# Kernel tuning notes

Measured on AMD Instinct MI355X. Metric: run time of the kernel, lower is better.

The kernel has to match this reference:

```python
import jax, jax.numpy as jnp
import numpy as np

DIM = 192
HEADS = 4
EPS = 1e-12  # F.normalize default eps


def setup_inputs() -> dict:
    key = jax.random.key(0)
    ks = jax.random.split(key, 5)
    b, c, h, w = 8, DIM, 128, 128
    x = jax.random.normal(ks[0], (b, c, h, w), dtype=jnp.float32)
    w_qkv = jax.random.normal(ks[1], (3 * DIM, DIM, 1, 1), dtype=jnp.float32) * (1.0 / np.sqrt(DIM))
    w_dw = jax.random.normal(ks[2], (3 * DIM, 1, 3, 3), dtype=jnp.float32) * (1.0 / 3.0)
    w_proj = jax.random.normal(ks[3], (DIM, DIM, 1, 1), dtype=jnp.float32) * (1.0 / np.sqrt(DIM))
    temperature = jnp.ones((HEADS, 1, 1), dtype=jnp.float32)
    return {"x": x, "w_qkv": w_qkv, "w_dw": w_dw, "w_proj": w_proj, "temperature": temperature}


def _conv1x1(x, w):
    # x: [b,c,h,w], w: [o,c,1,1] -> [b,o,h,w]
    return jnp.einsum('bchw,oc->bohw', x, w[:, :, 0, 0])


def _dwconv3x3(x, w):
    # depthwise 3x3, padding=1; x: [b,C,h,w], w: [C,1,3,3]
    C = x.shape[1]
    return jax.lax.conv_general_dilated(
        x, w, window_strides=(1, 1), padding=((1, 1), (1, 1)),
        dimension_numbers=('NCHW', 'OIHW', 'NCHW'), feature_group_count=C)


def _l2norm(x):
    n = jnp.linalg.norm(x, axis=-1, keepdims=True)
    return x / jnp.maximum(n, EPS)


def reference(x, w_qkv, w_dw, w_proj, temperature):
    b, c, h, w = x.shape
    head = HEADS
    ch = c // head  # channels per head
    qkv = _dwconv3x3(_conv1x1(x, w_qkv), w_dw)  # [b, 3c, h, w]
    q, k, v = jnp.split(qkv, 3, axis=1)  # each [b, c, h, w]

    def to_heads(t):
        # b (head ch) h w -> b head h (ch w)
        t = t.reshape(b, head, ch, h, w)
        return t.transpose(0, 1, 3, 2, 4).reshape(b, head, h, ch * w)

    q1 = _l2norm(to_heads(q))
    k1 = _l2norm(to_heads(k))
    v1 = to_heads(v)
    # attn over height dim: [b, head, h, h]
    attn = jax.nn.softmax(jnp.einsum('bhif,bhjf->bhij', q1, k1) * temperature[None], axis=-1)
    out = jnp.einsum('bhij,bhjf->bhif', attn, v1)  # [b, head, h, ch*w]
    # b head h (ch w) -> b (head ch) h w
    out = out.reshape(b, head, h, ch, w).transpose(0, 1, 3, 2, 4).reshape(b, c, h, w)
    return _conv1x1(out, w_proj)
```

## Files before the change

kernel.cpp:

```cpp
#include <hip/hip_runtime.h>
#include <hip/hip_bf16.h>

#define BB 8
#define CC 192
#define C3 576
#define NH 4
#define CH 48
#define HH 128
#define WW 128
#define HW 16384
#define FF 6144

typedef short s16x8 __attribute__((ext_vector_type(8)));
typedef float f32x4 __attribute__((ext_vector_type(4)));

constexpr size_t SPM = 32ull * 128 * 128;

constexpr size_t OFF_XT  = 0;
constexpr size_t SZ_XT   = (size_t)BB * HW * CC * 2;
constexpr size_t OFF_WQ  = OFF_XT + SZ_XT;
constexpr size_t SZ_WQ   = (size_t)C3 * CC * 2;
constexpr size_t OFF_WP  = OFF_WQ + SZ_WQ;
constexpr size_t SZ_WP   = (size_t)CC * CC * 2;
constexpr size_t OFF_RAW = OFF_WP + SZ_WP;
constexpr size_t SZ_RAW  = (size_t)BB * C3 * HW * 2;
constexpr size_t OFF_DW  = OFF_RAW + SZ_RAW;
constexpr size_t OFF_SP  = OFF_DW + SZ_RAW;
constexpr size_t OFF_ATB = OFF_SP + 8 * SPM * 4;
constexpr size_t OFF_RQ  = OFF_ATB + 32ull * 128 * 128 * 2;
constexpr size_t OFF_RK  = OFF_RQ + 32 * 128 * 4;
constexpr size_t OFF_PS  = OFF_SP;

__device__ __forceinline__ void store_out(__hip_bfloat16* p, float v) { *p = __float2bfloat16(v); }
__device__ __forceinline__ void store_out(float* p, float v) { *p = v; }

__device__ __forceinline__ short bf16bits(float v) {
  __hip_bfloat16 t = __float2bfloat16(v);
  return *reinterpret_cast<short*>(&t);
}
__device__ __forceinline__ float b2f(short u) {
  union { unsigned int i; float f; } x;
  x.i = ((unsigned int)(unsigned short)u) << 16;
  return x.f;
}

__device__ __forceinline__ void gload16(const void* g, void* l) {
  __builtin_amdgcn_global_load_lds((const __attribute__((address_space(1))) unsigned int*)g,
                                   (__attribute__((address_space(3))) unsigned int*)l, 16, 0, 0);
}

__global__ __launch_bounds__(256) void k_cvt_t(const float* __restrict__ in,
                                               __hip_bfloat16* __restrict__ outT) {
  const int p0 = blockIdx.x * 64;
  const int c0 = blockIdx.y * 32;
  const int b = blockIdx.z;
  __shared__ float t[32][65];
  const float* ib = in + (size_t)b * CC * HW;
  const int tid = threadIdx.x;
  {
    const int c = tid >> 3, pl = (tid & 7) * 8;
    const float* s = ib + (size_t)(c0 + c) * HW + p0 + pl;
#pragma unroll
    for (int j = 0; j < 8; ++j) t[c][pl + j] = s[j];
  }
  __syncthreads();
  {
    const int pl = tid >> 2, cl = (tid & 3) * 8;
    __hip_bfloat16* d = outT + (size_t)b * HW * CC + (size_t)(p0 + pl) * CC + c0 + cl;
#pragma unroll
    for (int j = 0; j < 8; ++j) d[j] = __float2bfloat16(t[cl + j][pl]);
  }
}

__global__ __launch_bounds__(256) void k_cvt_w(const float* __restrict__ in,
                                               __hip_bfloat16* __restrict__ out, int n) {
  const int i = blockIdx.x * 256 + threadIdx.x;
  if (i < n) out[i] = __float2bfloat16(in[i]);
}

template <int M, typename OutT>
__global__ __launch_bounds__(256) void k_gemm(const __hip_bfloat16* __restrict__ xT,
                                              const __hip_bfloat16* __restrict__ Wb,
                                              OutT* __restrict__ out) {
  const int pBase = blockIdx.x * 128;
  const int mBase = blockIdx.y * 192;
  const int b = blockIdx.z;
  __shared__ __hip_bfloat16 Al[6144];
  __shared__ __hip_bfloat16 Bl[4096];
  const int tid = threadIdx.x;
  const int wave = tid >> 6, lane = tid & 63;
  const int wm = wave >> 1, wn = wave & 1;
  const __hip_bfloat16* xb = xT + (size_t)b * HW * CC;
  char* Alc = (char*)Al;
  char* Blc = (char*)Bl;
  f32x4 acc[6][4] = {};

  for (int k0 = 0; k0 < CC; k0 += 32) {
#pragma unroll
    for (int is = 0; is < 3; ++is) {
      const int ci = is * 256 + tid;
      const int row = ci & 15, kg = (ci >> 4) & 3, mf = ci >> 6;
      gload16(Wb + (size_t)(mBase + mf * 16 + row) * CC + k0 + kg * 8,
              Alc + is * 4096 + wave * 1024);
    }
#pragma unroll
    for (int is = 0; is < 2; ++is) {
      const int ci = is * 256 + tid;
      const int col = ci & 15, kg = (ci >> 4) & 3, nf = ci >> 6;
      gload16(xb + (size_t)(pBase + nf * 16 + col) * CC + k0 + kg * 8,
              Blc + is * 4096 + wave * 1024);
    }
    __syncthreads();
    s16x8 a[6], bf[4];
#pragma unroll
    for (int i = 0; i < 6; ++i) a[i] = *(const s16x8*)(Alc + ((wm * 6 + i) << 10) + (lane << 4));
#pragma unroll
    for (int j = 0; j < 4; ++j) bf[j] = *(const s16x8*)(Blc + ((wn * 4 + j) << 10) + (lane << 4));
#pragma unroll
    for (int i = 0; i < 6; ++i)
#pragma unroll
      for (int j = 0; j < 4; ++j)
        acc[i][j] = __builtin_amdgcn_mfma_f32_16x16x32_bf16(a[i], bf[j], acc[i][j], 0, 0, 0);
    __syncthreads();
  }
  OutT* ob = out + (size_t)b * M * HW;
  const int r0 = (lane >> 4) * 4, cl = lane & 15;
#pragma unroll
  for (int i = 0; i < 6; ++i) {
    const int o = mBase + (wm * 6 + i) * 16 + r0;
#pragma unroll
    for (int j = 0; j < 4; ++j) {
      const int p = pBase + (wn * 4 + j) * 16 + cl;
      OutT* dst = ob + (size_t)o * HW + p;
#pragma unroll
      for (int r = 0; r < 4; ++r) store_out(dst + (size_t)r * HW, acc[i][j][r]);
    }
  }
}

__global__ __launch_bounds__(256) void k_dwconv(const __hip_bfloat16* __restrict__ in,
                                                const float* __restrict__ wdw,
                                                __hip_bfloat16* __restrict__ out,
                                                __hip_bfloat16* __restrict__ vt,
                                                float* __restrict__ psum) {
  const int h0 = blockIdx.x * 32;
  const int c = blockIdx.y;
  const int b = blockIdx.z;
  __shared__ __hip_bfloat16 IN[34][152];
  __shared__ char TR[8192];
  const int tid = threadIdx.x;
  const __hip_bfloat16* src = in + ((size_t)b * C3 + c) * HW;
  if (tid < 68) {
    const int r = tid >> 1, col = (tid & 1) ? 136 : 0;
    *(s16x8*)(&IN[r][col]) = (s16x8){};
  }
#pragma unroll
  for (int it = 0; it < 3; ++it) {
    const int vi = it * 256 + tid;
    if (vi < 544) {
      const int r = vi >> 4, w8 = vi & 15;
      const int hg = h0 - 1 + r;
      s16x8 v = {};
      if (hg >= 0 && hg < HH) v = *(const s16x8*)(src + (size_t)hg * WW + w8 * 8);
      *(s16x8*)(&IN[r][8 + w8 * 8]) = v;
    }
  }
  const float* wp = wdw + c * 9;
  float wgt[9];
#pragma unroll
  for (int q = 0; q < 9; ++q) wgt[q] = wp[q];
  __syncthreads();

  const int hl = tid >> 3, w0 = (tid & 7) * 16;
  float res[16] = {};
#pragma unroll
  for (int dh = 0; dh < 3; ++dh) {
    const __hip_bfloat16* rp = &IN[hl + dh][0];
    const s16x8 v0 = *(const s16x8*)(rp + w0);
    const s16x8 v1 = *(const s16x8*)(rp + w0 + 8);
    const s16x8 v2 = *(const s16x8*)(rp + w0 + 16);
    const s16x8 v3 = *(const s16x8*)(rp + w0 + 24);
    float rv[18];
    rv[0] = b2f(v0[7]);
#pragma unroll
    for (int e = 0; e < 8; ++e) rv[1 + e] = b2f(v1[e]);
#pragma unroll
    for (int e = 0; e < 8; ++e) rv[9 + e] = b2f(v2[e]);
    rv[17] = b2f(v3[0]);
    const float wa = wgt[dh * 3], wb = wgt[dh * 3 + 1], wc = wgt[dh * 3 + 2];
#pragma unroll
    for (int ww = 0; ww < 16; ++ww)
      res[ww] += rv[ww] * wa + rv[ww + 1] * wb + rv[ww + 2] * wc;
  }
  if (c < 2 * CC) {
    short pk[16];
#pragma unroll
    for (int ww = 0; ww < 16; ++ww) pk[ww] = bf16bits(res[ww]);
    __hip_bfloat16* dst = out + ((size_t)b * C3 + c) * HW + (size_t)(h0 + hl) * WW + w0;
    *(s16x8*)dst = *(const s16x8*)pk;
    *(s16x8*)(dst + 8) = *(const s16x8*)(pk + 8);
    float ss = 0.f;
#pragma unroll
    for (int ww = 0; ww < 16; ++ww) ss += res[ww] * res[ww];
#pragma unroll
    for (int off = 4; off > 0; off >>= 1) ss += __shfl_down(ss, off);
    if ((tid & 7) == 0) psum[((size_t)b * HH + h0 + hl) * 384 + c] = ss;
  } else {
    const int rel = c - 2 * CC;
    const int hd = rel / CH, ch = rel - hd * CH;
#pragma unroll
    for (int ww = 0; ww < 16; ++ww) {
      const int w = w0 + ww;
      const int blk = ((w << 2) + (hl >> 3)) ^ ((w >> 3) & 3);
      *(short*)(TR + (blk << 4) + ((hl & 7) << 1)) = bf16bits(res[ww]);
    }
    __syncthreads();
    const int w = tid >> 1, hf = tid & 1;
    short ot[16];
#pragma unroll
    for (int j = 0; j < 2; ++j) {
      const int hh = hf * 16 + j * 8;
      const int blk = ((w << 2) + (hh >> 3)) ^ ((w >> 3) & 3);
      *(s16x8*)(ot + j * 8) = *(const s16x8*)(TR + (blk << 4));
    }
    __hip_bfloat16* vd = vt + ((size_t)(b * NH + hd) * FF + (size_t)ch * WW + w) * HH + h0 + hf * 16;
    *(s16x8*)vd = *(const s16x8*)ot;
    *(s16x8*)(vd + 8) = *(const s16x8*)(ot + 8);
  }
}

__global__ __launch_bounds__(64) void k_norms2(const float* __restrict__ psum,
                                               float* __restrict__ rq, float* __restrict__ rk) {
  const int i = blockIdx.x;
  const int hd = blockIdx.y;
  const int b = blockIdx.z & 7;
  const int which = blockIdx.z >> 3;
  const int lane = threadIdx.x;
  float s = 0.f;
  if (lane < 48) s = psum[((size_t)b * HH + i) * 384 + which * CC + hd * CH + lane];
#pragma unroll
  for (int off = 32; off > 0; off >>= 1) s += __shfl_down(s, off);
  if (lane == 0) {
    const float n = sqrtf(s);
    float* dst = which ? rk : rq;
    dst[(b * NH + hd) * HH + i] = 1.f / fmaxf(n, 1e-12f);
  }
}

__global__ __launch_bounds__(256) void k_qkm(const __hip_bfloat16* __restrict__ dw,
                                             float* __restrict__ sp) {
  const int ks = blockIdx.x;
  const int bh = blockIdx.y;
  const int b = bh >> 2, hd = bh & 3;
  const __hip_bfloat16* qb = dw + ((size_t)b * C3 + hd * CH) * HW;
  const __hip_bfloat16* kb = dw + ((size_t)b * C3 + CC + hd * CH) * HW;
  __shared__ __hip_bfloat16 Al[4096];
  __shared__ __hip_bfloat16 Bl[4096];
  char* Alc = (char*)Al;
  char* Blc = (char*)Bl;
  const int tid = threadIdx.x, wave = tid >> 6, lane = tid & 63;
  const int wm = wave >> 1, wn = wave & 1;
  f32x4 acc[4][4] = {};
  for (int chunk = 0; chunk < 24; ++chunk) {
    const int ch = ks * 6 + (chunk >> 2);
    const int w0 = (chunk & 3) * 32;
#pragma unroll
    for (int is = 0; is < 2; ++is) {
      const int ci = is * 256 + tid;
      const int row = ci & 15, kg = (ci >> 4) & 3, mf = ci >> 6;
      gload16(qb + (size_t)ch * HW + (mf * 16 + row) * WW + w0 + kg * 8,
              Alc + is * 4096 + wave * 1024);
    }
#pragma unroll
    for (int is = 0; is < 2; ++is) {
      const int ci = is * 256 + tid;
      const int col = ci & 15, kg = (ci >> 4) & 3, nf = ci >> 6;
      gload16(kb + (size_t)ch * HW + (nf * 16 + col) * WW + w0 + kg * 8,
              Blc + is * 4096 + wave * 1024);
    }
    __syncthreads();
    s16x8 a[4], bf[4];
#pragma unroll
    for (int i = 0; i < 4; ++i) a[i] = *(const s16x8*)(Alc + ((wm * 4 + i) << 10) + (lane << 4));
#pragma unroll
    for (int j = 0; j < 4; ++j) bf[j] = *(const s16x8*)(Blc + ((wn * 4 + j) << 10) + (lane << 4));
#pragma unroll
    for (int i = 0; i < 4; ++i)
#pragma unroll
      for (int j = 0; j < 4; ++j)
        acc[i][j] = __builtin_amdgcn_mfma_f32_16x16x32_bf16(a[i], bf[j], acc[i][j], 0, 0, 0);
    __syncthreads();
  }
  float* o = sp + (size_t)ks * SPM + (size_t)bh * HH * HH;
  const int r0 = (lane >> 4) * 4, cl = lane & 15;
#pragma unroll
  for (int i = 0; i < 4; ++i)
#pragma unroll
    for (int j = 0; j < 4; ++j) {
      const int ii = wm * 64 + i * 16 + r0;
      const int jj = wn * 64 + j * 16 + cl;
#pragma unroll
      for (int r = 0; r < 4; ++r) o[(ii + r) * HH + jj] = acc[i][j][r];
    }
}

__global__ __launch_bounds__(64) void k_softmax(const float* __restrict__ sp,
                                                const float* __restrict__ rq,
                                                const float* __restrict__ rk,
                                                const float* __restrict__ temp,
                                                __hip_bfloat16* __restrict__ atb) {
  const int i = blockIdx.x;
  const int bh = blockIdx.y;
  const int hd = bh & 3;
  const int lane = threadIdx.x;
  const size_t rowoff = ((size_t)bh * HH + i) * HH;
  float s0 = 0.f, s1 = 0.f;
#pragma unroll
  for (int ks = 0; ks < 8; ++ks) {
    s0 += sp[ks * SPM + rowoff + lane];
    s1 += sp[ks * SPM + rowoff + lane + 64];
  }
  const float scale = rq[bh * HH + i] * temp[hd];
  s0 *= scale * rk[bh * HH + lane];
  s1 *= scale * rk[bh * HH + lane + 64];
  float m = fmaxf(s0, s1);
#pragma unroll
  for (int off = 32; off > 0; off >>= 1) m = fmaxf(m, __shfl_xor(m, off));
  const float e0 = expf(s0 - m), e1 = expf(s1 - m);
  float ssum = e0 + e1;
#pragma unroll
  for (int off = 32; off > 0; off >>= 1) ssum += __shfl_xor(ssum, off);
  const float inv = 1.f / ssum;
  atb[rowoff + lane] = __float2bfloat16(e0 * inv);
  atb[rowoff + lane + 64] = __float2bfloat16(e1 * inv);
}

__global__ __launch_bounds__(256) void k_pvm(const __hip_bfloat16* __restrict__ atb,
                                             const __hip_bfloat16* __restrict__ vt,
                                             __hip_bfloat16* __restrict__ pvout) {
  const int fs = blockIdx.x;
  const int bh = blockIdx.y;
  const __hip_bfloat16* ab = atb + (size_t)bh * HH * HH;
  const __hip_bfloat16* vb = vt + ((size_t)bh * FF + fs * 256) * HH;
  __shared__ __hip_bfloat16 Al[4096];
  __shared__ __hip_bfloat16 Bl[8192];
  char* Alc = (char*)Al;
  char* Blc = (char*)Bl;
  const int tid = threadIdx.x, wave = tid >> 6, lane = tid & 63;
  const int wm = wave >> 1, wn = wave & 1;
  f32x4 acc[4][8] = {};
  for (int kc = 0; kc < 4; ++kc) {
    const int kj0 = kc * 32;
#pragma unroll
    for (int is = 0; is < 2; ++is) {
      const int ci = is * 256 + tid;
      const int row = ci & 15, kg = (ci >> 4) & 3, mf = ci >> 6;
      gload16(ab + (size_t)(mf * 16 + row) * HH + kj0 + kg * 8,
              Alc + is * 4096 + wave * 1024);
    }
#pragma unroll
    for (int is = 0; is < 4; ++is) {
      const int ci = is * 256 + tid;
      const int col = ci & 15, kg = (ci >> 4) & 3, nf = ci >> 6;
      gload16(vb + (size_t)(nf * 16 + col) * HH + kj0 + kg * 8,
              Blc + is * 4096 + wave * 1024);
    }
    __syncthreads();
    s16x8 a[4], bf[8];
#pragma unroll
    for (int i = 0; i < 4; ++i) a[i] = *(const s16x8*)(Alc + ((wm * 4 + i) << 10) + (lane << 4));
#pragma unroll
    for (int j = 0; j < 8; ++j) bf[j] = *(const s16x8*)(Blc + ((wn * 8 + j) << 10) + (lane << 4));
#pragma unroll
    for (int i = 0; i < 4; ++i)
#pragma unroll
      for (int j = 0; j < 8; ++j)
        acc[i][j] = __builtin_amdgcn_mfma_f32_16x16x32_bf16(a[i], bf[j], acc[i][j], 0, 0, 0);
    __syncthreads();
  }
  __hip_bfloat16* ob = pvout + (size_t)bh * HH * FF;
  const int r0 = (lane >> 4) * 4, cl = lane & 15;
#pragma unroll
  for (int i = 0; i < 4; ++i)
#pragma unroll
    for (int j = 0; j < 8; ++j) {
      const int ii = wm * 64 + i * 16 + r0;
      const int f = fs * 256 + wn * 128 + j * 16 + cl;
#pragma unroll
      for (int r = 0; r < 4; ++r) ob[(size_t)(ii + r) * FF + f] = __float2bfloat16(acc[i][j][r]);
    }
}

__global__ __launch_bounds__(256) void k_proj(const __hip_bfloat16* __restrict__ pv,
                                              const __hip_bfloat16* __restrict__ Wp,
                                              float* __restrict__ out) {
  const int i = blockIdx.x;
  const int b = blockIdx.y;
  __shared__ __hip_bfloat16 Al[6144];
  __shared__ __hip_bfloat16 Braw[12288];
  __shared__ __hip_bfloat16 Bfrag[12288];
  char* Alc = (char*)Al;
  char* Brc = (char*)Braw;
  char* Bfc = (char*)Bfrag;
  const int tid = threadIdx.x, wave = tid >> 6, lane = tid & 63;
  const int wm = wave >> 1, wn = wave & 1;
  f32x4 acc[6][4] = {};
  for (int hf = 0; hf < 2; ++hf) {
#pragma unroll
    for (int it = 0; it < 6; ++it) {
      const int vi = it * 256 + tid;
      const int r = vi >> 4, w8 = vi & 15;
      const int hi = (r >= 48) ? 1 : 0;
      const int hd = hf * 2 + hi, ch = r - hi * 48;
      const s16x8 v = *(const s16x8*)(pv + ((size_t)(b * NH + hd) * HH + i) * FF + ch * 128 + w8 * 8);
      *(s16x8*)(Brc + r * 256 + ((w8 ^ (r & 15)) << 4)) = v;
    }
    __syncthreads();
#pragma unroll
    for (int it = 0; it < 6; ++it) {
      const int vi = it * 256 + tid;
      const int col = vi & 15, kg12 = (vi >> 4) % 12, nf = vi / 192;
      const int w = nf * 16 + col;
      short tmp[8];
#pragma unroll
      for (int e = 0; e < 8; ++e) {
        const int r = kg12 * 8 + e;
        tmp[e] = *(const short*)(Brc + r * 256 + (((w >> 3) ^ (r & 15)) << 4) + (w & 7) * 2);
      }
      const int kc = kg12 >> 2, kg = kg12 & 3;
      *(s16x8*)(Bfc + (((nf * 3 + kc) * 64 + kg * 16 + col) << 4)) = *(const s16x8*)tmp;
    }
    for (int kc = 0; kc < 3; ++kc) {
      const int c0 = hf * 96 + kc * 32;
#pragma unroll
      for (int is = 0; is < 3; ++is) {
        const int ci = is * 256 + tid;
        const int row = ci & 15, kg = (ci >> 4) & 3, mf = ci >> 6;
        gload16(Wp + (size_t)(mf * 16 + row) * CC + c0 + kg * 8,
                Alc + is * 4096 + wave * 1024);
      }
      __syncthreads();
      s16x8 a[6], bf[4];
#pragma unroll
      for (int mi = 0; mi < 6; ++mi)
        a[mi] = *(const s16x8*)(Alc + ((wm * 6 + mi) << 10) + (lane << 4));
#pragma unroll
      for (int j = 0; j < 4; ++j)
        bf[j] = *(const s16x8*)(Bfc + ((((wn * 4 + j) * 3 + kc) * 64 + lane) << 4));
#pragma unroll
      for (int mi = 0; mi < 6; ++mi)
#pragma unroll
        for (int j = 0; j < 4; ++j)
          acc[mi][j] = __builtin_amdgcn_mfma_f32_16x16x32_bf16(a[mi], bf[j], acc[mi][j], 0, 0, 0);
      __syncthreads();
    }
  }
  const int r0 = (lane >> 4) * 4, cl = lane & 15;
#pragma unroll
  for (int mi = 0; mi < 6; ++mi) {
    const int o = (wm * 6 + mi) * 16 + r0;
#pragma unroll
    for (int j = 0; j < 4; ++j) {
      const int w = (wn * 4 + j) * 16 + cl;
      float* dst = out + ((size_t)b * CC + o) * HW + i * 128 + w;
#pragma unroll
      for (int r = 0; r < 4; ++r) dst[(size_t)r * HW] = acc[mi][j][r];
    }
  }
}

extern "C" void kernel_launch(void* const* d_in, const int* in_sizes, int n_in,
                              void* d_out, int out_size, void* d_ws, size_t ws_size,
                              hipStream_t stream) {
  const float* x     = (const float*)d_in[0];
  const float* wqkv  = (const float*)d_in[1];
  const float* wdw   = (const float*)d_in[2];
  const float* wproj = (const float*)d_in[3];
  const float* temp  = (const float*)d_in[4];

  char* ws = (char*)d_ws;
  __hip_bfloat16* xTb    = (__hip_bfloat16*)(ws + OFF_XT);
  __hip_bfloat16* vt     = (__hip_bfloat16*)(ws + OFF_XT);
  __hip_bfloat16* Wq     = (__hip_bfloat16*)(ws + OFF_WQ);
  __hip_bfloat16* Wp     = (__hip_bfloat16*)(ws + OFF_WP);
  __hip_bfloat16* qkvraw = (__hip_bfloat16*)(ws + OFF_RAW);
  __hip_bfloat16* pvout  = (__hip_bfloat16*)(ws + OFF_RAW);
  __hip_bfloat16* qkvdw  = (__hip_bfloat16*)(ws + OFF_DW);
  float* sp    = (float*)(ws + OFF_SP);
  float* psum  = (float*)(ws + OFF_PS);
  __hip_bfloat16* atb = (__hip_bfloat16*)(ws + OFF_ATB);
  float* rq    = (float*)(ws + OFF_RQ);
  float* rk    = (float*)(ws + OFF_RK);

  k_cvt_w<<<dim3((C3 * CC + 255) / 256), 256, 0, stream>>>(wqkv, Wq, C3 * CC);
  k_cvt_w<<<dim3((CC * CC + 255) / 256), 256, 0, stream>>>(wproj, Wp, CC * CC);
  k_cvt_t<<<dim3(HW / 64, CC / 32, BB), 256, 0, stream>>>(x, xTb);
  k_gemm<C3, __hip_bfloat16><<<dim3(HW / 128, 3, BB), 256, 0, stream>>>(xTb, Wq, qkvraw);
  k_dwconv<<<dim3(HH / 32, C3, BB), 256, 0, stream>>>(qkvraw, wdw, qkvdw, vt, psum);
  k_norms2<<<dim3(HH, NH, 2 * BB), 64, 0, stream>>>(psum, rq, rk);
  k_qkm<<<dim3(8, 32), 256, 0, stream>>>(qkvdw, sp);
  k_softmax<<<dim3(HH, 32), 64, 0, stream>>>(sp, rq, rk, temp, atb);
  k_pvm<<<dim3(24, 32), 256, 0, stream>>>(atb, vt, pvout);
  k_proj<<<dim3(HH, BB), 256, 0, stream>>>(pvout, Wp, (float*)d_out);
}
```

Baseline: 284.8 us.

## Fuse input transpose/convert into QKV GEMM with double-buffered warp-specialized loads

```diff
diff --git a/kernel.cpp b/kernel.cpp
--- a/kernel.cpp
+++ b/kernel.cpp
@@ -31,9 +31,6 @@
 constexpr size_t OFF_RK  = OFF_RQ + 32 * 128 * 4;
 constexpr size_t OFF_PS  = OFF_SP;
 
-__device__ __forceinline__ void store_out(__hip_bfloat16* p, float v) { *p = __float2bfloat16(v); }
-__device__ __forceinline__ void store_out(float* p, float v) { *p = v; }
-
 __device__ __forceinline__ short bf16bits(float v) {
   __hip_bfloat16 t = __float2bfloat16(v);
   return *reinterpret_cast<short*>(&t);
@@ -49,91 +46,94 @@
                                    (__attribute__((address_space(3))) unsigned int*)l, 16, 0, 0);
 }
 
-__global__ __launch_bounds__(256) void k_cvt_t(const float* __restrict__ in,
-                                               __hip_bfloat16* __restrict__ outT) {
-  const int p0 = blockIdx.x * 64;
-  const int c0 = blockIdx.y * 32;
-  const int b = blockIdx.z;
-  __shared__ float t[32][65];
-  const float* ib = in + (size_t)b * CC * HW;
-  const int tid = threadIdx.x;
-  {
-    const int c = tid >> 3, pl = (tid & 7) * 8;
-    const float* s = ib + (size_t)(c0 + c) * HW + p0 + pl;
-#pragma unroll
-    for (int j = 0; j < 8; ++j) t[c][pl + j] = s[j];
-  }
-  __syncthreads();
-  {
-    const int pl = tid >> 2, cl = (tid & 3) * 8;
-    __hip_bfloat16* d = outT + (size_t)b * HW * CC + (size_t)(p0 + pl) * CC + c0 + cl;
-#pragma unroll
-    for (int j = 0; j < 8; ++j) d[j] = __float2bfloat16(t[cl + j][pl]);
-  }
-}
-
 __global__ __launch_bounds__(256) void k_cvt_w(const float* __restrict__ in,
                                                __hip_bfloat16* __restrict__ out, int n) {
   const int i = blockIdx.x * 256 + threadIdx.x;
   if (i < n) out[i] = __float2bfloat16(in[i]);
 }
 
-template <int M, typename OutT>
-__global__ __launch_bounds__(256) void k_gemm(const __hip_bfloat16* __restrict__ xT,
-                                              const __hip_bfloat16* __restrict__ Wb,
-                                              OutT* __restrict__ out) {
-  const int pBase = blockIdx.x * 128;
-  const int mBase = blockIdx.y * 192;
-  const int b = blockIdx.z;
-  __shared__ __hip_bfloat16 Al[6144];
-  __shared__ __hip_bfloat16 Bl[4096];
-  const int tid = threadIdx.x;
-  const int wave = tid >> 6, lane = tid & 63;
+__global__ __launch_bounds__(512, 4) void k_gemmx(const float* __restrict__ x,
+                                                  const __hip_bfloat16* __restrict__ Wb,
+                                                  __hip_bfloat16* __restrict__ out) {
+  const int pBase = blockIdx.x * 64;
+  const int b = blockIdx.y;
+  __shared__ __hip_bfloat16 Al[2][18432];
+  __shared__ __hip_bfloat16 Bf[2][2048];
+  const int tid = threadIdx.x, wave = tid >> 6, lane = tid & 63;
   const int wm = wave >> 1, wn = wave & 1;
-  const __hip_bfloat16* xb = xT + (size_t)b * HW * CC;
-  char* Alc = (char*)Al;
-  char* Blc = (char*)Bl;
-  f32x4 acc[6][4] = {};
-
-  for (int k0 = 0; k0 < CC; k0 += 32) {
-#pragma unroll
-    for (int is = 0; is < 3; ++is) {
-      const int ci = is * 256 + tid;
-      const int row = ci & 15, kg = (ci >> 4) & 3, mf = ci >> 6;
-      gload16(Wb + (size_t)(mBase + mf * 16 + row) * CC + k0 + kg * 8,
-              Alc + is * 4096 + wave * 1024);
-    }
-#pragma unroll
-    for (int is = 0; is < 2; ++is) {
-      const int ci = is * 256 + tid;
-      const int col = ci & 15, kg = (ci >> 4) & 3, nf = ci >> 6;
-      gload16(xb + (size_t)(pBase + nf * 16 + col) * CC + k0 + kg * 8,
-              Blc + is * 4096 + wave * 1024);
-    }
-    __syncthreads();
-    s16x8 a[6], bf[4];
-#pragma unroll
-    for (int i = 0; i < 6; ++i) a[i] = *(const s16x8*)(Alc + ((wm * 6 + i) << 10) + (lane << 4));
-#pragma unroll
-    for (int j = 0; j < 4; ++j) bf[j] = *(const s16x8*)(Blc + ((wn * 4 + j) << 10) + (lane << 4));
-#pragma unroll
-    for (int i = 0; i < 6; ++i)
-#pragma unroll
-      for (int j = 0; j < 4; ++j)
-        acc[i][j] = __builtin_amdgcn_mfma_f32_16x16x32_bf16(a[i], bf[j], acc[i][j], 0, 0, 0);
-    __syncthreads();
-  }
-  OutT* ob = out + (size_t)b * M * HW;
+  const float* xb = x + (size_t)b * CC * HW;
+  f32x4 acc[9][2] = {};
+  const bool isB = wave < 4;
+  const int col = tid & 15, kg = (tid >> 4) & 3, nf = (tid >> 6) & 3;
+  const float* xcol = xb + (size_t)(kg * 8) * HW + pBase + nf * 16 + col;
+  const int wa = wave - 4;
+  float xr[8];
+
+  if (isB) {
+#pragma unroll
+    for (int e = 0; e < 8; ++e) xr[e] = xcol[(size_t)e * HW];
+    short fr[8];
+#pragma unroll
+    for (int e = 0; e < 8; ++e) fr[e] = bf16bits(xr[e]);
+    *(s16x8*)((char*)Bf[0] + ((nf * 64 + kg * 16 + col) << 4)) = *(const s16x8*)fr;
+  } else {
+#pragma unroll
+    for (int it = 0; it < 9; ++it) {
+      const int base = wa * 576 + it * 64;
+      const int s = base + lane;
+      const int row = s & 15, kga = (s >> 4) & 3, mf = s >> 6;
+      gload16(Wb + (size_t)(mf * 16 + row) * CC + kga * 8, (char*)Al[0] + (base << 4));
+    }
+  }
+  __syncthreads();
+  for (int kc = 0; kc < 6; ++kc) {
+    const int cur = kc & 1, nx = cur ^ 1;
+    const int k1 = (kc + 1) * 32;
+    if (kc < 5) {
+      if (isB) {
+#pragma unroll
+        for (int e = 0; e < 8; ++e) xr[e] = xcol[(size_t)(k1 + e) * HW];
+      } else {
+#pragma unroll
+        for (int it = 0; it < 9; ++it) {
+          const int base = wa * 576 + it * 64;
+          const int s = base + lane;
+          const int row = s & 15, kga = (s >> 4) & 3, mf = s >> 6;
+          gload16(Wb + (size_t)(mf * 16 + row) * CC + k1 + kga * 8,
+                  (char*)Al[nx] + (base << 4));
+        }
+      }
+    }
+    s16x8 bfr[2];
+#pragma unroll
+    for (int j = 0; j < 2; ++j)
+      bfr[j] = *(const s16x8*)((char*)Bf[cur] + (((wn * 2 + j) * 64 + lane) << 4));
+#pragma unroll
+    for (int i = 0; i < 9; ++i) {
+      const s16x8 a = *(const s16x8*)((char*)Al[cur] + (((wm * 9 + i) * 64 + lane) << 4));
+#pragma unroll
+      for (int j = 0; j < 2; ++j)
+        acc[i][j] = __builtin_amdgcn_mfma_f32_16x16x32_bf16(a, bfr[j], acc[i][j], 0, 0, 0);
+    }
+    if (kc < 5 && isB) {
+      short fr[8];
+#pragma unroll
+      for (int e = 0; e < 8; ++e) fr[e] = bf16bits(xr[e]);
+      *(s16x8*)((char*)Bf[nx] + ((nf * 64 + kg * 16 + col) << 4)) = *(const s16x8*)fr;
+    }
+    __syncthreads();
+  }
+  __hip_bfloat16* ob = out + (size_t)b * C3 * HW;
   const int r0 = (lane >> 4) * 4, cl = lane & 15;
 #pragma unroll
-  for (int i = 0; i < 6; ++i) {
-    const int o = mBase + (wm * 6 + i) * 16 + r0;
-#pragma unroll
-    for (int j = 0; j < 4; ++j) {
-      const int p = pBase + (wn * 4 + j) * 16 + cl;
-      OutT* dst = ob + (size_t)o * HW + p;
-#pragma unroll
-      for (int r = 0; r < 4; ++r) store_out(dst + (size_t)r * HW, acc[i][j][r]);
+  for (int i = 0; i < 9; ++i) {
+    const int o = (wm * 9 + i) * 16 + r0;
+#pragma unroll
+    for (int j = 0; j < 2; ++j) {
+      const int pp = pBase + (wn * 2 + j) * 16 + cl;
+      __hip_bfloat16* dst = ob + (size_t)o * HW + pp;
+#pragma unroll
+      for (int r = 0; r < 4; ++r) dst[(size_t)r * HW] = __float2bfloat16(acc[i][j][r]);
     }
   }
 }
@@ -479,7 +479,6 @@
   const float* temp  = (const float*)d_in[4];
 
   char* ws = (char*)d_ws;
-  __hip_bfloat16* xTb    = (__hip_bfloat16*)(ws + OFF_XT);
   __hip_bfloat16* vt     = (__hip_bfloat16*)(ws + OFF_XT);
   __hip_bfloat16* Wq     = (__hip_bfloat16*)(ws + OFF_WQ);
   __hip_bfloat16* Wp     = (__hip_bfloat16*)(ws + OFF_WP);
@@ -494,8 +493,7 @@
 
   k_cvt_w<<<dim3((C3 * CC + 255) / 256), 256, 0, stream>>>(wqkv, Wq, C3 * CC);
   k_cvt_w<<<dim3((CC * CC + 255) / 256), 256, 0, stream>>>(wproj, Wp, CC * CC);
-  k_cvt_t<<<dim3(HW / 64, CC / 32, BB), 256, 0, stream>>>(x, xTb);
-  k_gemm<C3, __hip_bfloat16><<<dim3(HW / 128, 3, BB), 256, 0, stream>>>(xTb, Wq, qkvraw);
+  k_gemmx<<<dim3(HW / 64, BB), 512, 0, stream>>>(x, Wq, qkvraw);
   k_dwconv<<<dim3(HH / 32, C3, BB), 256, 0, stream>>>(qkvraw, wdw, qkvdw, vt, psum);
   k_norms2<<<dim3(HH, NH, 2 * BB), 64, 0, stream>>>(psum, rq, rk);
   k_qkm<<<dim3(8, 32), 256, 0, stream>>>(qkvdw, sp);
```

Result: slower. 390.8 us (+37.2%).

## Double-buffer LDS staging in GEMM kernels and stage QKV epilogue through LDS

Applied to the files above, without the earlier changes.

```diff
diff --git a/kernel.cpp b/kernel.cpp
--- a/kernel.cpp
+++ b/kernel.cpp
@@ -31,9 +31,6 @@
 constexpr size_t OFF_RK  = OFF_RQ + 32 * 128 * 4;
 constexpr size_t OFF_PS  = OFF_SP;
 
-__device__ __forceinline__ void store_out(__hip_bfloat16* p, float v) { *p = __float2bfloat16(v); }
-__device__ __forceinline__ void store_out(float* p, float v) { *p = v; }
-
 __device__ __forceinline__ short bf16bits(float v) {
   __hip_bfloat16 t = __float2bfloat16(v);
   return *reinterpret_cast<short*>(&t);
@@ -48,6 +45,8 @@
   __builtin_amdgcn_global_load_lds((const __attribute__((address_space(1))) unsigned int*)g,
                                    (__attribute__((address_space(3))) unsigned int*)l, 16, 0, 0);
 }
+
+__device__ __forceinline__ void vmdrain() { asm volatile("s_waitcnt vmcnt(0)" ::: "memory"); }
 
 __global__ __launch_bounds__(256) void k_cvt_t(const float* __restrict__ in,
                                                __hip_bfloat16* __restrict__ outT) {
@@ -72,30 +71,30 @@
   }
 }
 
-__global__ __launch_bounds__(256) void k_cvt_w(const float* __restrict__ in,
-                                               __hip_bfloat16* __restrict__ out, int n) {
+__global__ __launch_bounds__(256) void k_cvt_w2(const float* __restrict__ in1, int n1,
+                                                const float* __restrict__ in2, int n2,
+                                                __hip_bfloat16* __restrict__ out) {
   const int i = blockIdx.x * 256 + threadIdx.x;
-  if (i < n) out[i] = __float2bfloat16(in[i]);
-}
-
-template <int M, typename OutT>
+  if (i < n1) out[i] = __float2bfloat16(in1[i]);
+  else if (i < n1 + n2) out[i] = __float2bfloat16(in2[i - n1]);
+}
+
 __global__ __launch_bounds__(256) void k_gemm(const __hip_bfloat16* __restrict__ xT,
                                               const __hip_bfloat16* __restrict__ Wb,
-                                              OutT* __restrict__ out) {
+                                              __hip_bfloat16* __restrict__ out) {
   const int pBase = blockIdx.x * 128;
   const int mBase = blockIdx.y * 192;
   const int b = blockIdx.z;
-  __shared__ __hip_bfloat16 Al[6144];
-  __shared__ __hip_bfloat16 Bl[4096];
+  __shared__ char smem[52224];
   const int tid = threadIdx.x;
   const int wave = tid >> 6, lane = tid & 63;
   const int wm = wave >> 1, wn = wave & 1;
   const __hip_bfloat16* xb = xT + (size_t)b * HW * CC;
-  char* Alc = (char*)Al;
-  char* Blc = (char*)Bl;
   f32x4 acc[6][4] = {};
 
-  for (int k0 = 0; k0 < CC; k0 += 32) {
+  auto stage = [&](int k0, int buf) {
+    char* Alc = smem + buf * 12288;
+    char* Blc = smem + 24576 + buf * 8192;
 #pragma unroll
     for (int is = 0; is < 3; ++is) {
       const int ci = is * 256 + tid;
@@ -110,7 +109,16 @@
       gload16(xb + (size_t)(pBase + nf * 16 + col) * CC + k0 + kg * 8,
               Blc + is * 4096 + wave * 1024);
     }
-    __syncthreads();
+  };
+
+  stage(0, 0);
+  vmdrain();
+  __syncthreads();
+  for (int kc = 0; kc < 6; ++kc) {
+    const int cur = kc & 1;
+    if (kc < 5) stage((kc + 1) * 32, cur ^ 1);
+    char* Alc = smem + cur * 12288;
+    char* Blc = smem + 24576 + cur * 8192;
     s16x8 a[6], bf[4];
 #pragma unroll
     for (int i = 0; i < 6; ++i) a[i] = *(const s16x8*)(Alc + ((wm * 6 + i) << 10) + (lane << 4));
@@ -121,20 +129,29 @@
 #pragma unroll
       for (int j = 0; j < 4; ++j)
         acc[i][j] = __builtin_amdgcn_mfma_f32_16x16x32_bf16(a[i], bf[j], acc[i][j], 0, 0, 0);
+    vmdrain();
     __syncthreads();
   }
-  OutT* ob = out + (size_t)b * M * HW;
+  short* E = (short*)smem;
   const int r0 = (lane >> 4) * 4, cl = lane & 15;
 #pragma unroll
   for (int i = 0; i < 6; ++i) {
-    const int o = mBase + (wm * 6 + i) * 16 + r0;
+    const int row = (wm * 6 + i) * 16 + r0;
 #pragma unroll
     for (int j = 0; j < 4; ++j) {
-      const int p = pBase + (wn * 4 + j) * 16 + cl;
-      OutT* dst = ob + (size_t)o * HW + p;
-#pragma unroll
-      for (int r = 0; r < 4; ++r) store_out(dst + (size_t)r * HW, acc[i][j][r]);
-    }
+      const int col = (wn * 4 + j) * 16 + cl;
+#pragma unroll
+      for (int r = 0; r < 4; ++r) E[(row + r) * 136 + col] = bf16bits(acc[i][j][r]);
+    }
+  }
+  __syncthreads();
+  __hip_bfloat16* ob = out + (size_t)b * C3 * HW + pBase;
+#pragma unroll
+  for (int it = 0; it < 12; ++it) {
+    const int vi = it * 256 + tid;
+    const int row = vi >> 4, c8 = (vi & 15) * 8;
+    const s16x8 v = *(const s16x8*)(E + row * 136 + c8);
+    *(s16x8*)(ob + (size_t)(mBase + row) * HW + c8) = v;
   }
 }
 
@@ -254,16 +271,17 @@
   const int b = bh >> 2, hd = bh & 3;
   const __hip_bfloat16* qb = dw + ((size_t)b * C3 + hd * CH) * HW;
   const __hip_bfloat16* kb = dw + ((size_t)b * C3 + CC + hd * CH) * HW;
-  __shared__ __hip_bfloat16 Al[4096];
-  __shared__ __hip_bfloat16 Bl[4096];
-  char* Alc = (char*)Al;
-  char* Blc = (char*)Bl;
+  __shared__ __hip_bfloat16 Al[2][4096];
+  __shared__ __hip_bfloat16 Bl[2][4096];
   const int tid = threadIdx.x, wave = tid >> 6, lane = tid & 63;
   const int wm = wave >> 1, wn = wave & 1;
   f32x4 acc[4][4] = {};
-  for (int chunk = 0; chunk < 24; ++chunk) {
+
+  auto stage = [&](int chunk, int buf) {
     const int ch = ks * 6 + (chunk >> 2);
     const int w0 = (chunk & 3) * 32;
+    char* Alc = (char*)Al[buf];
+    char* Blc = (char*)Bl[buf];
 #pragma unroll
     for (int is = 0; is < 2; ++is) {
       const int ci = is * 256 + tid;
@@ -278,7 +296,16 @@
       gload16(kb + (size_t)ch * HW + (nf * 16 + col) * WW + w0 + kg * 8,
               Blc + is * 4096 + wave * 1024);
     }
-    __syncthreads();
+  };
+
+  stage(0, 0);
+  vmdrain();
+  __syncthreads();
+  for (int chunk = 0; chunk < 24; ++chunk) {
+    const int cur = chunk & 1;
+    if (chunk < 23) stage(chunk + 1, cur ^ 1);
+    char* Alc = (char*)Al[cur];
+    char* Blc = (char*)Bl[cur];
     s16x8 a[4], bf[4];
 #pragma unroll
     for (int i = 0; i < 4; ++i) a[i] = *(const s16x8*)(Alc + ((wm * 4 + i) << 10) + (lane << 4));
@@ -289,6 +316,7 @@
 #pragma unroll
       for (int j = 0; j < 4; ++j)
         acc[i][j] = __builtin_amdgcn_mfma_f32_16x16x32_bf16(a[i], bf[j], acc[i][j], 0, 0, 0);
+    vmdrain();
     __syncthreads();
   }
   float* o = sp + (size_t)ks * SPM + (size_t)bh * HH * HH;
@@ -342,15 +370,16 @@
   const int bh = blockIdx.y;
   const __hip_bfloat16* ab = atb + (size_t)bh * HH * HH;
   const __hip_bfloat16* vb = vt + ((size_t)bh * FF + fs * 256) * HH;
-  __shared__ __hip_bfloat16 Al[4096];
-  __shared__ __hip_bfloat16 Bl[8192];
-  char* Alc = (char*)Al;
-  char* Blc = (char*)Bl;
+  __shared__ __hip_bfloat16 Al[2][4096];
+  __shared__ __hip_bfloat16 Bl[2][8192];
   const int tid = threadIdx.x, wave = tid >> 6, lane = tid & 63;
   const int wm = wave >> 1, wn = wave & 1;
   f32x4 acc[4][8] = {};
-  for (int kc = 0; kc < 4; ++kc) {
+
+  auto stage = [&](int kc, int buf) {
     const int kj0 = kc * 32;
+    char* Alc = (char*)Al[buf];
+    char* Blc = (char*)Bl[buf];
 #pragma unroll
     for (int is = 0; is < 2; ++is) {
       const int ci = is * 256 + tid;
@@ -365,7 +394,16 @@
       gload16(vb + (size_t)(nf * 16 + col) * HH + kj0 + kg * 8,
               Blc + is * 4096 + wave * 1024);
     }
-    __syncthreads();
+  };
+
+  stage(0, 0);
+  vmdrain();
+  __syncthreads();
+  for (int kc = 0; kc < 4; ++kc) {
+    const int cur = kc & 1;
+    if (kc < 3) stage(kc + 1, cur ^ 1);
+    char* Alc = (char*)Al[cur];
+    char* Blc = (char*)Bl[cur];
     s16x8 a[4], bf[8];
 #pragma unroll
     for (int i = 0; i < 4; ++i) a[i] = *(const s16x8*)(Alc + ((wm * 4 + i) << 10) + (lane << 4));
@@ -376,6 +414,7 @@
 #pragma unroll
       for (int j = 0; j < 8; ++j)
         acc[i][j] = __builtin_amdgcn_mfma_f32_16x16x32_bf16(a[i], bf[j], acc[i][j], 0, 0, 0);
+    vmdrain();
     __syncthreads();
   }
   __hip_bfloat16* ob = pvout + (size_t)bh * HH * FF;
@@ -439,6 +478,7 @@
         gload16(Wp + (size_t)(mf * 16 + row) * CC + c0 + kg * 8,
                 Alc + is * 4096 + wave * 1024);
       }
+      vmdrain();
       __syncthreads();
       s16x8 a[6], bf[4];
 #pragma unroll
@@ -492,10 +532,9 @@
   float* rq    = (float*)(ws + OFF_RQ);
   float* rk    = (float*)(ws + OFF_RK);
 
-  k_cvt_w<<<dim3((C3 * CC + 255) / 256), 256, 0, stream>>>(wqkv, Wq, C3 * CC);
-  k_cvt_w<<<dim3((CC * CC + 255) / 256), 256, 0, stream>>>(wproj, Wp, CC * CC);
+  k_cvt_w2<<<dim3((C3 * CC + CC * CC + 255) / 256), 256, 0, stream>>>(wqkv, C3 * CC, wproj, CC * CC, Wq);
   k_cvt_t<<<dim3(HW / 64, CC / 32, BB), 256, 0, stream>>>(x, xTb);
-  k_gemm<C3, __hip_bfloat16><<<dim3(HW / 128, 3, BB), 256, 0, stream>>>(xTb, Wq, qkvraw);
+  k_gemm<<<dim3(HW / 128, 3, BB), 256, 0, stream>>>(xTb, Wq, qkvraw);
   k_dwconv<<<dim3(HH / 32, C3, BB), 256, 0, stream>>>(qkvraw, wdw, qkvdw, vt, psum);
   k_norms2<<<dim3(HH, NH, 2 * BB), 64, 0, stream>>>(psum, rq, rk);
   k_qkm<<<dim3(8, 32), 256, 0, stream>>>(qkvdw, sp);
```

Result: faster. 279.1 us (-2.0%).
